# Kernel optimization log

Hardware: AMD Instinct MI355X
Metric: run time of the kernel (lower is better)

Reference implementation:

```python
import jax, jax.numpy as jnp
import numpy as np

B, T, IN, H, NL = 64, 256, 64, 768, 2
LU, OUT = 256, 1
INPUT_SCALE = 1.5
OUTPUT_SCALE = 70.0
STD = 0.001  # nn.init.normal_(p, std=0.001) on all LSTM params


def setup_inputs() -> dict:
    key = jax.random.key(0)
    ks = jax.random.split(key, 16)
    inp = {"x": jax.random.normal(ks[0], (B, T, IN), jnp.float32)}
    dims = [IN, H]
    for l in range(NL):
        d = dims[l]
        inp[f"Wih{l}"] = (jax.random.normal(ks[1 + 4 * l], (4 * H, d)) * STD).astype(jnp.float32)
        inp[f"Whh{l}"] = (jax.random.normal(ks[2 + 4 * l], (4 * H, H)) * STD).astype(jnp.float32)
        inp[f"bih{l}"] = (jax.random.normal(ks[3 + 4 * l], (4 * H,)) * STD).astype(jnp.float32)
        inp[f"bhh{l}"] = (jax.random.normal(ks[4 + 4 * l], (4 * H,)) * STD).astype(jnp.float32)
    # MLP head (torch default-ish small init)
    inp["W1"] = (jax.random.normal(ks[9], (LU, H)) * (1.0 / np.sqrt(H))).astype(jnp.float32)
    inp["b1"] = jnp.zeros((LU,), jnp.float32)
    inp["W2"] = (jax.random.normal(ks[10], (OUT, LU)) * (1.0 / np.sqrt(LU))).astype(jnp.float32)
    inp["b2"] = jnp.zeros((OUT,), jnp.float32)
    return inp


def _lstm_layer(x, Wih, Whh, bih, bhh):
    # x: (B, T, D) -> hidden sequence (B, T, H). PyTorch gate order: i, f, g, o.
    b = x.shape[0]
    h = Whh.shape[1]
    # precompute input contributions for all timesteps: (B, T, 4H)
    xg = jnp.einsum('btd,gd->btg', x, Wih) + bih + bhh

    def step(carry, xt):
        hp, cp = carry
        gates = xt + hp @ Whh.T  # (B, 4H)
        i, f, g, o = jnp.split(gates, 4, axis=-1)
        c = jax.nn.sigmoid(f) * cp + jax.nn.sigmoid(i) * jnp.tanh(g)
        hn = jax.nn.sigmoid(o) * jnp.tanh(c)
        return (hn, c), hn

    h0 = jnp.zeros((b, h), x.dtype)
    (_, _), hs = jax.lax.scan(step, (h0, h0), xg.transpose(1, 0, 2))
    return hs.transpose(1, 0, 2)  # (B, T, H)


def reference(x, Wih0, Whh0, bih0, bhh0, Wih1, Whh1, bih1, bhh1, W1, b1, W2, b2):
    xs = x / INPUT_SCALE
    h1 = _lstm_layer(xs, Wih0, Whh0, bih0, bhh0)
    h2 = _lstm_layer(h1, Wih1, Whh1, bih1, bhh1)
    last = h2[:, -1, :]                       # (B, H)
    z = jax.nn.soft_sign(last @ W1.T + b1)    # Softsign: x / (1 + |x|)
    pred = (z @ W2.T + b2) * OUTPUT_SCALE     # (B, OUT)
    return pred[:, None, :]                   # unsqueeze(1) -> (B, 1, OUT)
```

## Files before the change

kernel.cpp:

```cpp
#include <hip/hip_runtime.h>
#include <hip/hip_bf16.h>


#define B_  64
#define T_  256
#define IN_ 64
#define H_  768
#define G_  3072
#define K0_ 832
#define K1_ 1536
#define NWG0 96
#define NWG  192
#define CB_  96
#define SLOT_ (CB_ * 64 * 8)

typedef __bf16 bf16_t;
typedef bf16_t bf16x8 __attribute__((ext_vector_type(8)));
typedef float  f32x4  __attribute__((ext_vector_type(4)));

__device__ __forceinline__ unsigned short f2bf(float f) {
    union { float f; unsigned u; } v; v.f = f;
    unsigned r = v.u + 0x7FFFu + ((v.u >> 16) & 1u);
    return (unsigned short)(r >> 16);
}
__device__ __forceinline__ float sigm(float x) {
    return 1.0f / (1.0f + expf(-x));
}
__device__ __forceinline__ void st_llc_u32(unsigned* p, unsigned v) {
    asm volatile("global_store_dword %0, %1, off sc1" :: "v"(p), "v"(v) : "memory");
}
#define MFMA16(a, b, c) __builtin_amdgcn_mfma_f32_16x16x32_bf16((a), (b), (c), 0, 0, 0)

__global__ __launch_bounds__(256) void prep_kernel(
    const float* __restrict__ x,
    const float* __restrict__ Wih0, const float* __restrict__ Whh0,
    const float* __restrict__ bih0, const float* __restrict__ bhh0,
    const float* __restrict__ Wih1, const float* __restrict__ Whh1,
    const float* __restrict__ bih1, const float* __restrict__ bhh1,
    unsigned short* __restrict__ xsT,
    unsigned short* __restrict__ W0cat,
    unsigned short* __restrict__ W1cat,
    float* __restrict__ bias0, float* __restrict__ bias1,
    int* __restrict__ ctrs)
{
    int i = blockIdx.x * blockDim.x + threadIdx.x;
    int stride = gridDim.x * blockDim.x;
    for (int j = i; j < B_ * T_ * IN_; j += stride) {
        int b = j >> 14;
        int t = (j >> 6) & (T_ - 1);
        int k = j & (IN_ - 1);
        xsT[(((size_t)t * B_) + b) * IN_ + k] = f2bf(x[j] * (1.0f / 1.5f));
    }
    for (int j = i; j < G_ * IN_; j += stride) {
        int r = j >> 6; int k = j & 63;
        W0cat[(size_t)r * K0_ + k] = f2bf(Wih0[j]);
    }
    for (int j = i; j < G_ * H_; j += stride) {
        int r = j / H_; int k = j - r * H_;
        W0cat[(size_t)r * K0_ + IN_ + k] = f2bf(Whh0[j]);
        W1cat[(size_t)r * K1_ + k]       = f2bf(Wih1[j]);
        W1cat[(size_t)r * K1_ + H_ + k]  = f2bf(Whh1[j]);
    }
    for (int j = i; j < G_; j += stride) {
        bias0[j] = bih0[j] + bhh0[j];
        bias1[j] = bih1[j] + bhh1[j];
    }
    for (int j = i; j < 512; j += stride) ctrs[j] = 0;
}

__global__ __launch_bounds__(256) void lstm_persistent(
    const unsigned short* __restrict__ xsT,
    const unsigned short* __restrict__ W0cat,
    const unsigned short* __restrict__ W1cat,
    const float* __restrict__ bias0, const float* __restrict__ bias1,
    unsigned short* __restrict__ h1ring,
    unsigned short* __restrict__ h2ring,
    float* __restrict__ hf32,
    int* __restrict__ ctrs)
{
    __shared__ unsigned short ldsb[4][16][8];

    const int tid  = threadIdx.x;
    const int lane = tid & 63;
    const int wave = tid >> 6;
    const int wg   = blockIdx.x;
    const bool isL1 = (wg >= NWG0);
    const int cb   = isL1 ? (wg - NWG0) : wg;
    const int c0   = cb * 8;
    const int frow = lane & 15;
    const int q    = lane >> 4;
    const int kof  = q * 8;
    const int m0   = wave * 16;

    int* ctr0 = &ctrs[0];
    int* ctr1 = &ctrs[256];

    const unsigned short* Wc = isL1 ? W1cat : W0cat;
    const int Kc = isL1 ? K1_ : K0_;
    int q0 = frow >> 3,        col0 = c0 + (frow & 7);
    int q1 = 2 + (frow >> 3),  col1 = c0 + (frow & 7);
    const unsigned short* Bp0 = Wc + (size_t)(q0 * H_ + col0) * Kc + kof;
    const unsigned short* Bp1 = Wc + (size_t)(q1 * H_ + col1) * Kc + kof;

    const float* bias = isL1 ? bias1 : bias0;
    const bool lowhalf = (lane & 15) < 8;
    const int ecol = c0 + (lane & 7);
    float bi = 0.f, bff = 0.f, bg = 0.f, bo = 0.f;
    if (lowhalf) {
        bi  = bias[0 * H_ + ecol];
        bff = bias[1 * H_ + ecol];
        bg  = bias[2 * H_ + ecol];
        bo  = bias[3 * H_ + ecol];
    }
    float creg[4] = {0.f, 0.f, 0.f, 0.f};

    const size_t aoff = (size_t)q * 512 + (size_t)(m0 + frow) * 8;
    const size_t stoff_e = (size_t)cb * 512 + (size_t)(m0 + (lane >> 2)) * 8
                         + (size_t)(lane & 3) * 2;

    if (!isL1) {
        for (int s = 0; s < T_; ++s) {
            f32x4 acc0 = {0.f, 0.f, 0.f, 0.f};
            f32x4 acc1 = {0.f, 0.f, 0.f, 0.f};
            {
                const unsigned short* xsp =
                    xsT + ((size_t)s * B_ + m0 + frow) * IN_ + kof;
                #pragma unroll
                for (int ki = 0; ki < 2; ki++) {
                    bf16x8 a  = *(const bf16x8*)(xsp + ki * 32);
                    bf16x8 b0 = *(const bf16x8*)(Bp0 + ki * 32);
                    bf16x8 b1 = *(const bf16x8*)(Bp1 + ki * 32);
                    acc0 = MFMA16(a, b0, acc0);
                    acc1 = MFMA16(a, b1, acc1);
                }
            }
            if (s > 0) {
                if (tid == 0) {
                    while (__hip_atomic_load(ctr0, __ATOMIC_RELAXED,
                                             __HIP_MEMORY_SCOPE_AGENT) < NWG0 * s)
                        __builtin_amdgcn_s_sleep(1);
                }
                __syncthreads();
                const unsigned short* hr = h1ring + (size_t)(s - 1) * SLOT_ + aoff;
                #pragma unroll
                for (int kj = 0; kj < 24; kj++) {
                    bf16x8 a  = *(const bf16x8*)(hr + kj * 2048);
                    bf16x8 b0 = *(const bf16x8*)(Bp0 + (kj + 2) * 32);
                    bf16x8 b1 = *(const bf16x8*)(Bp1 + (kj + 2) * 32);
                    acc0 = MFMA16(a, b0, acc0);
                    acc1 = MFMA16(a, b1, acc1);
                }
            }
            f32x4 pacc0, pacc1;
            #pragma unroll
            for (int j = 0; j < 4; j++) {
                pacc0[j] = __shfl_xor(acc0[j], 8);
                pacc1[j] = __shfl_xor(acc1[j], 8);
            }
            if (lowhalf) {
                #pragma unroll
                for (int j = 0; j < 4; j++) {
                    float pi = acc0[j]  + bi;
                    float pf = pacc0[j] + bff;
                    float pg = acc1[j]  + bg;
                    float po = pacc1[j] + bo;
                    float cn = sigm(pf) * creg[j] + sigm(pi) * tanhf(pg);
                    float hn = sigm(po) * tanhf(cn);
                    creg[j] = cn;
                    ldsb[wave][q * 4 + j][lane & 7] = f2bf(hn);
                }
            }
            unsigned v = ((const unsigned*)&ldsb[wave][0][0])[lane];
            st_llc_u32((unsigned*)(h1ring + (size_t)s * SLOT_ + stoff_e), v);
            __syncthreads();
            if (tid == 0) atomicAdd(ctr0, 1);
        }
    } else {
        for (int s = 1; s <= T_; ++s) {
            const int t = s - 1;
            if (tid == 0) {
                while (__hip_atomic_load(ctr0, __ATOMIC_RELAXED,
                                         __HIP_MEMORY_SCOPE_AGENT) < NWG0 * s)
                    __builtin_amdgcn_s_sleep(1);
            }
            if (tid == 64 && t > 0) {
                while (__hip_atomic_load(ctr1, __ATOMIC_RELAXED,
                                         __HIP_MEMORY_SCOPE_AGENT) < NWG0 * (s - 1))
                    __builtin_amdgcn_s_sleep(1);
            }
            __syncthreads();
            f32x4 acc0 = {0.f, 0.f, 0.f, 0.f};
            f32x4 acc1 = {0.f, 0.f, 0.f, 0.f};
            const unsigned short* h1r = h1ring + (size_t)t * SLOT_ + aoff;
            #pragma unroll
            for (int ki = 0; ki < 24; ki++) {
                bf16x8 a  = *(const bf16x8*)(h1r + ki * 2048);
                bf16x8 b0 = *(const bf16x8*)(Bp0 + ki * 32);
                bf16x8 b1 = *(const bf16x8*)(Bp1 + ki * 32);
                acc0 = MFMA16(a, b0, acc0);
                acc1 = MFMA16(a, b1, acc1);
            }
            if (t > 0) {
                const unsigned short* h2r = h2ring + (size_t)(t - 1) * SLOT_ + aoff;
                #pragma unroll
                for (int ki = 0; ki < 24; ki++) {
                    bf16x8 a  = *(const bf16x8*)(h2r + ki * 2048);
                    bf16x8 b0 = *(const bf16x8*)(Bp0 + (ki + 24) * 32);
                    bf16x8 b1 = *(const bf16x8*)(Bp1 + (ki + 24) * 32);
                    acc0 = MFMA16(a, b0, acc0);
                    acc1 = MFMA16(a, b1, acc1);
                }
            }
            f32x4 pacc0, pacc1;
            #pragma unroll
            for (int j = 0; j < 4; j++) {
                pacc0[j] = __shfl_xor(acc0[j], 8);
                pacc1[j] = __shfl_xor(acc1[j], 8);
            }
            if (lowhalf) {
                #pragma unroll
                for (int j = 0; j < 4; j++) {
                    int row = m0 + q * 4 + j;
                    float pi = acc0[j]  + bi;
                    float pf = pacc0[j] + bff;
                    float pg = acc1[j]  + bg;
                    float po = pacc1[j] + bo;
                    float cn = sigm(pf) * creg[j] + sigm(pi) * tanhf(pg);
                    float hn = sigm(po) * tanhf(cn);
                    creg[j] = cn;
                    ldsb[wave][q * 4 + j][lane & 7] = f2bf(hn);
                    if (t == T_ - 1) hf32[(size_t)row * H_ + ecol] = hn;
                }
            }
            unsigned v = ((const unsigned*)&ldsb[wave][0][0])[lane];
            st_llc_u32((unsigned*)(h2ring + (size_t)t * SLOT_ + stoff_e), v);
            __syncthreads();
            if (tid == 0) atomicAdd(ctr1, 1);
        }
    }
}

__global__ __launch_bounds__(256) void head_kernel(
    const float* __restrict__ hlast,
    const float* __restrict__ W1, const float* __restrict__ b1,
    const float* __restrict__ W2, const float* __restrict__ b2,
    float* __restrict__ out)
{
    __shared__ float hs[H_];
    __shared__ float partial[4];
    int b = blockIdx.x;
    int tid = threadIdx.x;
    for (int j = tid; j < H_; j += 256) hs[j] = hlast[(size_t)b * H_ + j];
    __syncthreads();
    float z = 0.f;
    const float* w = W1 + (size_t)tid * H_;
    for (int j = 0; j < H_; j++) z += hs[j] * w[j];
    z += b1[tid];
    z = z / (1.0f + fabsf(z));
    float p = z * W2[tid];
    #pragma unroll
    for (int off = 32; off > 0; off >>= 1) p += __shfl_down(p, off, 64);
    if ((tid & 63) == 0) partial[tid >> 6] = p;
    __syncthreads();
    if (tid == 0) {
        float s = partial[0] + partial[1] + partial[2] + partial[3];
        out[b] = (s + b2[0]) * 70.0f;
    }
}

extern "C" void kernel_launch(void* const* d_in, const int* in_sizes, int n_in,
                              void* d_out, int out_size, void* d_ws, size_t ws_size,
                              hipStream_t stream) {
    const float* x    = (const float*)d_in[0];
    const float* Wih0 = (const float*)d_in[1];
    const float* Whh0 = (const float*)d_in[2];
    const float* bih0 = (const float*)d_in[3];
    const float* bhh0 = (const float*)d_in[4];
    const float* Wih1 = (const float*)d_in[5];
    const float* Whh1 = (const float*)d_in[6];
    const float* bih1 = (const float*)d_in[7];
    const float* bhh1 = (const float*)d_in[8];
    const float* W1   = (const float*)d_in[9];
    const float* b1   = (const float*)d_in[10];
    const float* W2   = (const float*)d_in[11];
    const float* b2   = (const float*)d_in[12];
    float* out = (float*)d_out;

    char* w = (char*)d_ws;
    int* ctrs = (int*)w;                          w += 2048;
    unsigned short* h1ring = (unsigned short*)w;  w += (size_t)T_ * SLOT_ * 2;
    unsigned short* h2ring = (unsigned short*)w;  w += (size_t)T_ * SLOT_ * 2;
    unsigned short* xsT    = (unsigned short*)w;  w += (size_t)B_ * T_ * IN_ * 2;
    unsigned short* W0cat  = (unsigned short*)w;  w += (size_t)G_ * K0_ * 2;
    unsigned short* W1cat  = (unsigned short*)w;  w += (size_t)G_ * K1_ * 2;
    float* bias0 = (float*)w;                     w += G_ * 4;
    float* bias1 = (float*)w;                     w += G_ * 4;
    float* hf32  = (float*)w;                     w += (size_t)B_ * H_ * 4;

    prep_kernel<<<1024, 256, 0, stream>>>(x, Wih0, Whh0, bih0, bhh0,
                                          Wih1, Whh1, bih1, bhh1,
                                          xsT, W0cat, W1cat, bias0, bias1, ctrs);
    lstm_persistent<<<NWG, 256, 0, stream>>>(xsT, W0cat, W1cat, bias0, bias1,
                                             h1ring, h2ring, hf32, ctrs);
    head_kernel<<<B_, 256, 0, stream>>>(hf32, W1, b1, W2, b2, out);
}
```

Before: 3.658 ms.

## Split batch into independent groups with per-group counters and reorder layer-1 waits

Repartitions the persistent LSTM so each layer's 96 workgroups form 4 batch groups of 16 rows, each group with 24 workgroups covering 32 hidden columns. Each group synchronises only through its own step counter, so a workgroup waits on 24 peers rather than 96. The hidden-state ring becomes a plain row-major (B,H) layout. Layer 1 now does its recurrent h2 matmul before waiting on layer 0's output, overlapping that wait with compute. The trade-off is an extra __syncthreads per step for the cross-wave LDS staging, and each workgroup now loads weights for 32 columns across its four waves.

```diff
diff --git a/kernel.cpp b/kernel.cpp
--- a/kernel.cpp
+++ b/kernel.cpp
@@ -9,10 +9,11 @@
 #define G_  3072
 #define K0_ 832
 #define K1_ 1536
-#define NWG0 96
+#define NGRP 4
+#define NCW  24
+#define NWGL 96
 #define NWG  192
-#define CB_  96
-#define SLOT_ (CB_ * 64 * 8)
+#define SLOT_ (B_ * H_)
 
 typedef __bf16 bf16_t;
 typedef bf16_t bf16x8 __attribute__((ext_vector_type(8)));
@@ -65,7 +66,7 @@
         bias0[j] = bih0[j] + bhh0[j];
         bias1[j] = bih1[j] + bhh1[j];
     }
-    for (int j = i; j < 512; j += stride) ctrs[j] = 0;
+    for (int j = i; j < 2048; j += stride) ctrs[j] = 0;
 }
 
 __global__ __launch_bounds__(256) void lstm_persistent(
@@ -78,33 +79,34 @@
     float* __restrict__ hf32,
     int* __restrict__ ctrs)
 {
-    __shared__ unsigned short ldsb[4][16][8];
+    __shared__ unsigned short ldsb[16][32];
 
     const int tid  = threadIdx.x;
     const int lane = tid & 63;
     const int wave = tid >> 6;
     const int wg   = blockIdx.x;
-    const bool isL1 = (wg >= NWG0);
-    const int cb   = isL1 ? (wg - NWG0) : wg;
-    const int c0   = cb * 8;
+    const bool isL1 = (wg >= NWGL);
+    const int lwg  = isL1 ? (wg - NWGL) : wg;
+    const int g    = lwg / NCW;
+    const int c    = lwg % NCW;
+    const int c0w  = c * 32 + wave * 8;
     const int frow = lane & 15;
     const int q    = lane >> 4;
     const int kof  = q * 8;
-    const int m0   = wave * 16;
-
-    int* ctr0 = &ctrs[0];
-    int* ctr1 = &ctrs[256];
+
+    int* ctr0 = &ctrs[g * 64];
+    int* ctr1 = &ctrs[1024 + g * 64];
 
     const unsigned short* Wc = isL1 ? W1cat : W0cat;
     const int Kc = isL1 ? K1_ : K0_;
-    int q0 = frow >> 3,        col0 = c0 + (frow & 7);
-    int q1 = 2 + (frow >> 3),  col1 = c0 + (frow & 7);
-    const unsigned short* Bp0 = Wc + (size_t)(q0 * H_ + col0) * Kc + kof;
-    const unsigned short* Bp1 = Wc + (size_t)(q1 * H_ + col1) * Kc + kof;
+    const int q0 = frow >> 3;
+    const int colb = c0w + (frow & 7);
+    const unsigned short* Bp0 = Wc + (size_t)(q0 * H_ + colb) * Kc + kof;
+    const unsigned short* Bp1 = Wc + (size_t)((2 + q0) * H_ + colb) * Kc + kof;
 
     const float* bias = isL1 ? bias1 : bias0;
     const bool lowhalf = (lane & 15) < 8;
-    const int ecol = c0 + (lane & 7);
+    const int ecol = c0w + (lane & 7);
     float bi = 0.f, bff = 0.f, bg = 0.f, bo = 0.f;
     if (lowhalf) {
         bi  = bias[0 * H_ + ecol];
@@ -114,9 +116,11 @@
     }
     float creg[4] = {0.f, 0.f, 0.f, 0.f};
 
-    const size_t aoff = (size_t)q * 512 + (size_t)(m0 + frow) * 8;
-    const size_t stoff_e = (size_t)cb * 512 + (size_t)(m0 + (lane >> 2)) * 8
-                         + (size_t)(lane & 3) * 2;
+    const size_t aoff = (size_t)(g * 16 + frow) * H_ + kof;
+    const int srow = wave * 4 + (lane >> 4);
+    const int sword = lane & 15;
+    const size_t stoff = (size_t)(g * 16 + srow) * H_ + c * 32 + sword * 2;
+    const int ldsrd = srow * 16 + sword;
 
     if (!isL1) {
         for (int s = 0; s < T_; ++s) {
@@ -124,7 +128,7 @@
             f32x4 acc1 = {0.f, 0.f, 0.f, 0.f};
             {
                 const unsigned short* xsp =
-                    xsT + ((size_t)s * B_ + m0 + frow) * IN_ + kof;
+                    xsT + ((size_t)s * B_ + g * 16 + frow) * IN_ + kof;
                 #pragma unroll
                 for (int ki = 0; ki < 2; ki++) {
                     bf16x8 a  = *(const bf16x8*)(xsp + ki * 32);
@@ -137,14 +141,14 @@
             if (s > 0) {
                 if (tid == 0) {
                     while (__hip_atomic_load(ctr0, __ATOMIC_RELAXED,
-                                             __HIP_MEMORY_SCOPE_AGENT) < NWG0 * s)
+                                             __HIP_MEMORY_SCOPE_AGENT) < NCW * s)
                         __builtin_amdgcn_s_sleep(1);
                 }
                 __syncthreads();
                 const unsigned short* hr = h1ring + (size_t)(s - 1) * SLOT_ + aoff;
                 #pragma unroll
                 for (int kj = 0; kj < 24; kj++) {
-                    bf16x8 a  = *(const bf16x8*)(hr + kj * 2048);
+                    bf16x8 a  = *(const bf16x8*)(hr + kj * 32);
                     bf16x8 b0 = *(const bf16x8*)(Bp0 + (kj + 2) * 32);
                     bf16x8 b1 = *(const bf16x8*)(Bp1 + (kj + 2) * 32);
                     acc0 = MFMA16(a, b0, acc0);
@@ -167,46 +171,52 @@
                     float cn = sigm(pf) * creg[j] + sigm(pi) * tanhf(pg);
                     float hn = sigm(po) * tanhf(cn);
                     creg[j] = cn;
-                    ldsb[wave][q * 4 + j][lane & 7] = f2bf(hn);
-                }
-            }
-            unsigned v = ((const unsigned*)&ldsb[wave][0][0])[lane];
-            st_llc_u32((unsigned*)(h1ring + (size_t)s * SLOT_ + stoff_e), v);
+                    ldsb[q * 4 + j][wave * 8 + (lane & 7)] = f2bf(hn);
+                }
+            }
+            __syncthreads();
+            {
+                unsigned v = ((const unsigned*)&ldsb[0][0])[ldsrd];
+                st_llc_u32((unsigned*)(h1ring + (size_t)s * SLOT_ + stoff), v);
+            }
             __syncthreads();
             if (tid == 0) atomicAdd(ctr0, 1);
         }
     } else {
         for (int s = 1; s <= T_; ++s) {
             const int t = s - 1;
+            f32x4 acc0 = {0.f, 0.f, 0.f, 0.f};
+            f32x4 acc1 = {0.f, 0.f, 0.f, 0.f};
+            if (t > 0) {
+                if (tid == 0) {
+                    while (__hip_atomic_load(ctr1, __ATOMIC_RELAXED,
+                                             __HIP_MEMORY_SCOPE_AGENT) < NCW * t)
+                        __builtin_amdgcn_s_sleep(1);
+                }
+                __syncthreads();
+                const unsigned short* h2r = h2ring + (size_t)(t - 1) * SLOT_ + aoff;
+                #pragma unroll
+                for (int ki = 0; ki < 24; ki++) {
+                    bf16x8 a  = *(const bf16x8*)(h2r + ki * 32);
+                    bf16x8 b0 = *(const bf16x8*)(Bp0 + (ki + 24) * 32);
+                    bf16x8 b1 = *(const bf16x8*)(Bp1 + (ki + 24) * 32);
+                    acc0 = MFMA16(a, b0, acc0);
+                    acc1 = MFMA16(a, b1, acc1);
+                }
+            }
             if (tid == 0) {
                 while (__hip_atomic_load(ctr0, __ATOMIC_RELAXED,
-                                         __HIP_MEMORY_SCOPE_AGENT) < NWG0 * s)
+                                         __HIP_MEMORY_SCOPE_AGENT) < NCW * s)
                     __builtin_amdgcn_s_sleep(1);
             }
-            if (tid == 64 && t > 0) {
-                while (__hip_atomic_load(ctr1, __ATOMIC_RELAXED,
-                                         __HIP_MEMORY_SCOPE_AGENT) < NWG0 * (s - 1))
-                    __builtin_amdgcn_s_sleep(1);
-            }
-            __syncthreads();
-            f32x4 acc0 = {0.f, 0.f, 0.f, 0.f};
-            f32x4 acc1 = {0.f, 0.f, 0.f, 0.f};
-            const unsigned short* h1r = h1ring + (size_t)t * SLOT_ + aoff;
-            #pragma unroll
-            for (int ki = 0; ki < 24; ki++) {
-                bf16x8 a  = *(const bf16x8*)(h1r + ki * 2048);
-                bf16x8 b0 = *(const bf16x8*)(Bp0 + ki * 32);
-                bf16x8 b1 = *(const bf16x8*)(Bp1 + ki * 32);
-                acc0 = MFMA16(a, b0, acc0);
-                acc1 = MFMA16(a, b1, acc1);
-            }
-            if (t > 0) {
-                const unsigned short* h2r = h2ring + (size_t)(t - 1) * SLOT_ + aoff;
+            __syncthreads();
+            {
+                const unsigned short* h1r = h1ring + (size_t)t * SLOT_ + aoff;
                 #pragma unroll
                 for (int ki = 0; ki < 24; ki++) {
-                    bf16x8 a  = *(const bf16x8*)(h2r + ki * 2048);
-                    bf16x8 b0 = *(const bf16x8*)(Bp0 + (ki + 24) * 32);
-                    bf16x8 b1 = *(const bf16x8*)(Bp1 + (ki + 24) * 32);
+                    bf16x8 a  = *(const bf16x8*)(h1r + ki * 32);
+                    bf16x8 b0 = *(const bf16x8*)(Bp0 + ki * 32);
+                    bf16x8 b1 = *(const bf16x8*)(Bp1 + ki * 32);
                     acc0 = MFMA16(a, b0, acc0);
                     acc1 = MFMA16(a, b1, acc1);
                 }
@@ -220,7 +230,6 @@
             if (lowhalf) {
                 #pragma unroll
                 for (int j = 0; j < 4; j++) {
-                    int row = m0 + q * 4 + j;
                     float pi = acc0[j]  + bi;
                     float pf = pacc0[j] + bff;
                     float pg = acc1[j]  + bg;
@@ -228,12 +237,16 @@
                     float cn = sigm(pf) * creg[j] + sigm(pi) * tanhf(pg);
                     float hn = sigm(po) * tanhf(cn);
                     creg[j] = cn;
-                    ldsb[wave][q * 4 + j][lane & 7] = f2bf(hn);
-                    if (t == T_ - 1) hf32[(size_t)row * H_ + ecol] = hn;
-                }
-            }
-            unsigned v = ((const unsigned*)&ldsb[wave][0][0])[lane];
-            st_llc_u32((unsigned*)(h2ring + (size_t)t * SLOT_ + stoff_e), v);
+                    ldsb[q * 4 + j][wave * 8 + (lane & 7)] = f2bf(hn);
+                    if (t == T_ - 1)
+                        hf32[(size_t)(g * 16 + q * 4 + j) * H_ + ecol] = hn;
+                }
+            }
+            __syncthreads();
+            {
+                unsigned v = ((const unsigned*)&ldsb[0][0])[ldsrd];
+                st_llc_u32((unsigned*)(h2ring + (size_t)t * SLOT_ + stoff), v);
+            }
             __syncthreads();
             if (tid == 0) atomicAdd(ctr1, 1);
         }
@@ -287,7 +300,7 @@
     float* out = (float*)d_out;
 
     char* w = (char*)d_ws;
-    int* ctrs = (int*)w;                          w += 2048;
+    int* ctrs = (int*)w;                          w += 8192;
     unsigned short* h1ring = (unsigned short*)w;  w += (size_t)T_ * SLOT_ * 2;
     unsigned short* h2ring = (unsigned short*)w;  w += (size_t)T_ * SLOT_ * 2;
     unsigned short* xsT    = (unsigned short*)w;  w += (size_t)B_ * T_ * IN_ * 2;
```

After: 4.118 ms. 1.13x slower.

## Add spinning filler workgroups and fast exp2/rcp gate activations

Applied to the files above, without the earlier changes.

Launches 64 extra workgroups that only run an FMA loop until the layer-1 workgroups set a done flag. This seems meant to keep the remaining compute units busy so clocks or power state stay high while the latency-bound recurrence runs. It also replaces the expf/tanhf-based sigmoid and tanh with hardware exp2 and reciprocal approximations, which shortens the per-step elementwise tail at a small cost in accuracy. The filler blocks add power draw and assume every workgroup is co-resident; if they were not, the persistent kernel could deadlock.

```diff
diff --git a/kernel.cpp b/kernel.cpp
--- a/kernel.cpp
+++ b/kernel.cpp
@@ -10,7 +10,8 @@
 #define K0_ 832
 #define K1_ 1536
 #define NWG0 96
-#define NWG  192
+#define NWGC 192
+#define NWGT 256
 #define CB_  96
 #define SLOT_ (CB_ * 64 * 8)
 
@@ -23,13 +24,19 @@
     unsigned r = v.u + 0x7FFFu + ((v.u >> 16) & 1u);
     return (unsigned short)(r >> 16);
 }
-__device__ __forceinline__ float sigm(float x) {
-    return 1.0f / (1.0f + expf(-x));
+__device__ __forceinline__ float fast_sigm(float x) {
+    float e = __builtin_amdgcn_exp2f(-1.44269504f * x);
+    return __builtin_amdgcn_rcpf(1.0f + e);
+}
+__device__ __forceinline__ float fast_tanh(float x) {
+    float e = __builtin_amdgcn_exp2f(2.88539008f * x);
+    return (e - 1.0f) * __builtin_amdgcn_rcpf(e + 1.0f);
 }
 __device__ __forceinline__ void st_llc_u32(unsigned* p, unsigned v) {
     asm volatile("global_store_dword %0, %1, off sc1" :: "v"(p), "v"(v) : "memory");
 }
 #define MFMA16(a, b, c) __builtin_amdgcn_mfma_f32_16x16x32_bf16((a), (b), (c), 0, 0, 0)
+#define AGENT_LD(p) __hip_atomic_load((p), __ATOMIC_RELAXED, __HIP_MEMORY_SCOPE_AGENT)
 
 __global__ __launch_bounds__(256) void prep_kernel(
     const float* __restrict__ x,
@@ -65,7 +72,7 @@
         bias0[j] = bih0[j] + bhh0[j];
         bias1[j] = bih1[j] + bhh1[j];
     }
-    for (int j = i; j < 512; j += stride) ctrs[j] = 0;
+    for (int j = i; j < 2048; j += stride) ctrs[j] = 0;
 }
 
 __global__ __launch_bounds__(256) void lstm_persistent(
@@ -84,6 +91,23 @@
     const int lane = tid & 63;
     const int wave = tid >> 6;
     const int wg   = blockIdx.x;
+
+    if (wg >= NWGC) {
+        int* done = &ctrs[1536];
+        float a = 1.0f + (float)tid * 1e-7f;
+        const float bm = 1.0000001f, cm = 1e-9f;
+        for (;;) {
+            for (int i = 0; i < 2048; i++)
+                a = __builtin_fmaf(a, bm, cm);
+            asm volatile("" : "+v"(a));
+            int d = 0;
+            if (lane == 0) d = AGENT_LD(done);
+            d = __builtin_amdgcn_readfirstlane(d);
+            if (d != 0) break;
+        }
+        return;
+    }
+
     const bool isL1 = (wg >= NWG0);
     const int cb   = isL1 ? (wg - NWG0) : wg;
     const int c0   = cb * 8;
@@ -97,10 +121,9 @@
 
     const unsigned short* Wc = isL1 ? W1cat : W0cat;
     const int Kc = isL1 ? K1_ : K0_;
-    int q0 = frow >> 3,        col0 = c0 + (frow & 7);
-    int q1 = 2 + (frow >> 3),  col1 = c0 + (frow & 7);
+    int q0 = frow >> 3, col0 = c0 + (frow & 7);
     const unsigned short* Bp0 = Wc + (size_t)(q0 * H_ + col0) * Kc + kof;
-    const unsigned short* Bp1 = Wc + (size_t)(q1 * H_ + col1) * Kc + kof;
+    const unsigned short* Bp1 = Wc + (size_t)((2 + q0) * H_ + col0) * Kc + kof;
 
     const float* bias = isL1 ? bias1 : bias0;
     const bool lowhalf = (lane & 15) < 8;
@@ -136,8 +159,7 @@
             }
             if (s > 0) {
                 if (tid == 0) {
-                    while (__hip_atomic_load(ctr0, __ATOMIC_RELAXED,
-                                             __HIP_MEMORY_SCOPE_AGENT) < NWG0 * s)
+                    while (AGENT_LD(ctr0) < NWG0 * s)
                         __builtin_amdgcn_s_sleep(1);
                 }
                 __syncthreads();
@@ -164,8 +186,8 @@
                     float pf = pacc0[j] + bff;
                     float pg = acc1[j]  + bg;
                     float po = pacc1[j] + bo;
-                    float cn = sigm(pf) * creg[j] + sigm(pi) * tanhf(pg);
-                    float hn = sigm(po) * tanhf(cn);
+                    float cn = fast_sigm(pf) * creg[j] + fast_sigm(pi) * fast_tanh(pg);
+                    float hn = fast_sigm(po) * fast_tanh(cn);
                     creg[j] = cn;
                     ldsb[wave][q * 4 + j][lane & 7] = f2bf(hn);
                 }
@@ -179,13 +201,11 @@
         for (int s = 1; s <= T_; ++s) {
             const int t = s - 1;
             if (tid == 0) {
-                while (__hip_atomic_load(ctr0, __ATOMIC_RELAXED,
-                                         __HIP_MEMORY_SCOPE_AGENT) < NWG0 * s)
+                while (AGENT_LD(ctr0) < NWG0 * s)
                     __builtin_amdgcn_s_sleep(1);
             }
             if (tid == 64 && t > 0) {
-                while (__hip_atomic_load(ctr1, __ATOMIC_RELAXED,
-                                         __HIP_MEMORY_SCOPE_AGENT) < NWG0 * (s - 1))
+                while (AGENT_LD(ctr1) < NWG0 * t)
                     __builtin_amdgcn_s_sleep(1);
             }
             __syncthreads();
@@ -225,8 +245,8 @@
                     float pf = pacc0[j] + bff;
                     float pg = acc1[j]  + bg;
                     float po = pacc1[j] + bo;
-                    float cn = sigm(pf) * creg[j] + sigm(pi) * tanhf(pg);
-                    float hn = sigm(po) * tanhf(cn);
+                    float cn = fast_sigm(pf) * creg[j] + fast_sigm(pi) * fast_tanh(pg);
+                    float hn = fast_sigm(po) * fast_tanh(cn);
                     creg[j] = cn;
                     ldsb[wave][q * 4 + j][lane & 7] = f2bf(hn);
                     if (t == T_ - 1) hf32[(size_t)row * H_ + ecol] = hn;
@@ -237,6 +257,7 @@
             __syncthreads();
             if (tid == 0) atomicAdd(ctr1, 1);
         }
+        if (tid == 0) st_llc_u32((unsigned*)&ctrs[1536], 1u);
     }
 }
 
@@ -287,7 +308,7 @@
     float* out = (float*)d_out;
 
     char* w = (char*)d_ws;
-    int* ctrs = (int*)w;                          w += 2048;
+    int* ctrs = (int*)w;                          w += 8192;
     unsigned short* h1ring = (unsigned short*)w;  w += (size_t)T_ * SLOT_ * 2;
     unsigned short* h2ring = (unsigned short*)w;  w += (size_t)T_ * SLOT_ * 2;
     unsigned short* xsT    = (unsigned short*)w;  w += (size_t)B_ * T_ * IN_ * 2;
@@ -300,7 +321,7 @@
     prep_kernel<<<1024, 256, 0, stream>>>(x, Wih0, Whh0, bih0, bhh0,
                                           Wih1, Whh1, bih1, bhh1,
                                           xsT, W0cat, W1cat, bias0, bias1, ctrs);
-    lstm_persistent<<<NWG, 256, 0, stream>>>(xsT, W0cat, W1cat, bias0, bias1,
-                                             h1ring, h2ring, hf32, ctrs);
+    lstm_persistent<<<NWGT, 256, 0, stream>>>(xsT, W0cat, W1cat, bias0, bias1,
+                                              h1ring, h2ring, hf32, ctrs);
     head_kernel<<<B_, 256, 0, stream>>>(hf32, W1, b1, W2, b2, out);
 }
```

New measurement: 3.237 ms. 1.13x faster.
